# Optimization experiments

Measured on AMD Instinct MI355X. Metric: run time of the kernel, lower is better.

## Reference

```python
import jax, jax.numpy as jnp
import numpy as np

B, N, D, R = 2, 256, 128, 32

def _sh_l1(r):
    # e3nn-style component-normalized l=1 spherical harmonics of unit vectors
    return jnp.sqrt(3.0) * r

def _sh_l2(r):
    x, y, z = r[..., 0], r[..., 1], r[..., 2]
    c = jnp.sqrt(15.0)
    return jnp.stack([
        c * x * y,
        c * y * z,
        0.5 * jnp.sqrt(5.0) * (3.0 * z * z - 1.0),  # x^2+y^2+z^2 = 1
        c * x * z,
        0.5 * c * (x * x - y * y),
    ], axis=-1)

def _radial(rbf, w1, b1, w2, b2):
    h = rbf @ w1 + b1
    return (h * jax.nn.sigmoid(h)) @ w2 + b2  # Linear -> SiLU -> Linear

def _layernorm(x, g, b, eps=1e-5):
    m = jnp.mean(x, axis=-1, keepdims=True)
    v = jnp.var(x, axis=-1, keepdims=True)
    return (x - m) * jax.lax.rsqrt(v + eps) * g + b

def setup_inputs() -> dict:
    key = jax.random.key(0)
    ks = iter(jax.random.split(key, 40))
    def nrm(shape, s=1.0):
        return jax.random.normal(next(ks), shape, dtype=jnp.float32) * s
    r_hat = nrm((B, N, N, 3))
    r_hat = r_hat / (jnp.linalg.norm(r_hat, axis=-1, keepdims=True) + 1e-9)
    inp = {
        'node_s': nrm((B, N, D)),
        'node_v': nrm((B, N, 3, D)),
        'node_t': nrm((B, N, 5, D)),
        'rbf': jax.random.uniform(next(ks), (B, N, N, R), dtype=jnp.float32),
        'r_hat': r_hat,
        'mask': jnp.ones((B, N, N), dtype=jnp.float32),
    }
    s1, s2 = 1.0 / np.sqrt(R), 1.0 / np.sqrt(D)
    for p in ('r0', 'r1', 'r2', 'r110'):
        inp[p + '_w1'] = nrm((R, D), s1)
        inp[p + '_b1'] = jnp.zeros((D,), jnp.float32)
        inp[p + '_w2'] = nrm((D, D), s2)
        inp[p + '_b2'] = jnp.zeros((D,), jnp.float32)
    inp['src_w'] = nrm((D, D), s2)
    inp['ln_g'] = jnp.ones((D,), jnp.float32)
    inp['ln_b'] = jnp.zeros((D,), jnp.float32)
    inp['out_w'] = nrm((D, D), s2)
    inp['out_b'] = jnp.zeros((D,), jnp.float32)
    inp['v_scale'] = jnp.ones((D,), jnp.float32)
    inp['t_scale'] = jnp.ones((D,), jnp.float32)
    return inp

def reference(node_s, node_v, node_t, rbf, r_hat, mask,
              r0_w1, r0_b1, r0_w2, r0_b2,
              r1_w1, r1_b1, r1_w2, r1_b2,
              r2_w1, r2_b1, r2_w2, r2_b2,
              r110_w1, r110_b1, r110_w2, r110_b2,
              src_w, ln_g, ln_b, out_w, out_b, v_scale, t_scale):
    h = node_s @ src_w                               # (B,N,D)
    h_j = h[:, None, :, :] * mask[..., None]         # (B,N,N,D): h_j[b,i,j]=h[b,j]*mask[b,i,j]
    Y1 = _sh_l1(r_hat)                               # (B,N,N,3)
    Y2 = _sh_l2(r_hat)                               # (B,N,N,5)

    msg_s = jnp.sum(h_j * _radial(rbf, r0_w1, r0_b1, r0_w2, r0_b2), axis=2)  # (B,N,D)
    delta_v = jnp.einsum('bijd,bijc->bicd',
                         h_j * _radial(rbf, r1_w1, r1_b1, r1_w2, r1_b2), Y1) * v_scale
    delta_t = jnp.einsum('bijd,bijc->bicd',
                         h_j * _radial(rbf, r2_w1, r2_b1, r2_w2, r2_b2), Y2) * t_scale

    # v_j[b,i,j] = node_v[b,i] (per the torch unsqueeze(2).expand)
    dot_vY1 = jnp.einsum('bicd,bijc->bijd', node_v, Y1)                      # (B,N,N,D)
    msg_s_from_v = jnp.sum(dot_vY1 * _radial(rbf, r110_w1, r110_b1, r110_w2, r110_b2)
                           * mask[..., None], axis=2)                        # (B,N,D)

    delta_s = _layernorm(msg_s + msg_s_from_v, ln_g, ln_b) @ out_w + out_b
    return (delta_s, delta_v, delta_t)
```

## Files before the change

kernel.cpp:

```cpp
#include <hip/hip_runtime.h>

#define Bb 2
#define Nn 256
#define Dd 128
#define Rr 32

typedef unsigned short u16;
typedef unsigned int   u32;
typedef __attribute__((ext_vector_type(8))) short bf16x8;
typedef __attribute__((ext_vector_type(4))) short bf16x4;
typedef __attribute__((ext_vector_type(4))) float f32x4;
typedef __attribute__((ext_vector_type(2))) u32   u32x2;
typedef __attribute__((ext_vector_type(4))) u32   u32x4;

__device__ u16 g_w1t[4*Dd*Rr];
__device__ u16 g_w2t[4*Dd*Dd];

__device__ __forceinline__ short f2bfs(float f){
  u32 u = __float_as_uint(f);
  u += 0x7FFFu + ((u >> 16) & 1u);
  return (short)(u >> 16);
}
__device__ __forceinline__ u16 f2bf(float f){
  u32 u = __float_as_uint(f);
  u += 0x7FFFu + ((u >> 16) & 1u);
  return (u16)(u >> 16);
}
__device__ __forceinline__ u32 cvtpk(float a, float b){
  u32 r;
  asm("v_cvt_pk_bf16_f32 %0, %1, %2" : "=v"(r) : "v"(a), "v"(b));
  return r;
}
__device__ __forceinline__ int swz(int j){
  return (j&3) | ((((j>>2)^(j>>3))&1)<<2);
}

__global__ __launch_bounds__(128) void prep_kernel(
    const float* __restrict__ node_s, const float* __restrict__ src_w,
    const float* __restrict__ r0w1, const float* __restrict__ r1w1,
    const float* __restrict__ r2w1, const float* __restrict__ r3w1,
    const float* __restrict__ r0w2, const float* __restrict__ r1w2,
    const float* __restrict__ r2w2, const float* __restrict__ r3w2,
    float* __restrict__ h_out)
{
  const int bx = blockIdx.x;
  const int t  = threadIdx.x;
  if (bx < Bb*Nn){
    __shared__ float s_row[Dd];
    s_row[t] = node_s[(size_t)bx*Dd + t];
    __syncthreads();
    float acc = 0.f;
    #pragma unroll 8
    for (int k=0;k<Dd;k++) acc += s_row[k]*src_w[k*Dd + t];
    h_out[(size_t)bx*Dd + t] = acc;
  } else {
    const int kb = bx - Bb*Nn;
    const int p  = kb >> 3, sl = kb & 7;
    const float* W1 = (p==0)?r0w1:(p==1)?r1w1:(p==2)?r2w1:r3w1;
    const float* W2 = (p==0)?r0w2:(p==1)?r1w2:(p==2)?r2w2:r3w2;
    u16* W1T = g_w1t + p*Dd*Rr;
    u16* W2T = g_w2t + p*Dd*Dd;
    #pragma unroll
    for (int it=0; it<4; it++){
      int in = sl*512 + it*128 + t;
      W1T[(in & 127)*Rr + (in >> 7)] = f2bf(W1[in]);
    }
    #pragma unroll
    for (int it=0; it<16; it++){
      int in = sl*2048 + it*128 + t;
      W2T[(in & 127)*Dd + (in >> 7)] = f2bf(W2[in]);
    }
  }
}

__global__ __launch_bounds__(512,4) void se3_mfma9(
    const float* __restrict__ node_v,
    const float* __restrict__ rbf,
    const float* __restrict__ r_hat,
    const float* __restrict__ maskp,
    const float* __restrict__ r0b1, const float* __restrict__ r0b2,
    const float* __restrict__ r1b1, const float* __restrict__ r1b2,
    const float* __restrict__ r2b1, const float* __restrict__ r2b2,
    const float* __restrict__ r3b1, const float* __restrict__ r3b2,
    const float* __restrict__ ln_g, const float* __restrict__ ln_b,
    const float* __restrict__ out_w, const float* __restrict__ out_b,
    const float* __restrict__ v_scale, const float* __restrict__ t_scale,
    const float* __restrict__ h_ws,
    float* __restrict__ out_s, float* __restrict__ out_v, float* __restrict__ out_t)
{
  __shared__ u16   s_rbf[Nn*36];
  __shared__ u16   s_hid[2*64*128];
  __shared__ u16   s_YT[10*264];
  __shared__ u16   s_Y1r[3*264];
  __shared__ float s_red[16*130];
  __shared__ float s_msg[Dd];
  __shared__ float s_xn[Dd];
  __shared__ float s_part[4*Dd];
  __shared__ float s_mv[2];

  const int tid  = threadIdx.x;
  const int bi   = blockIdx.x;
  const int b    = bi >> 8;
  const int lane = tid & 63;
  const int w    = tid >> 6;
  const int q    = lane >> 4;
  const int cc   = lane & 15;
  const int mpair= w & 1;
  const int dgrp = w >> 1;
  const int dbase= dgrp*32;

  if (tid < Nn){
    int j = tid;
    size_t pidx = (size_t)bi*Nn + j;
    float mk = maskp[pidx];
    float x = r_hat[pidx*3+0];
    float y = r_hat[pidx*3+1];
    float z = r_hat[pidx*3+2];
    const float SQ3=1.7320508075688772f;
    const float C15=3.8729833462074170f;
    const float C5H=1.1180339887498949f;
    float y1a=SQ3*x, y1b=SQ3*y, y1c=SQ3*z;
    s_YT[0*264+j]=f2bf(mk);
    s_YT[1*264+j]=f2bf(y1a*mk);
    s_YT[2*264+j]=f2bf(y1b*mk);
    s_YT[3*264+j]=f2bf(y1c*mk);
    s_YT[4*264+j]=f2bf(C15*x*y*mk);
    s_YT[5*264+j]=f2bf(C15*y*z*mk);
    s_YT[6*264+j]=f2bf(C5H*(3.f*z*z-1.f)*mk);
    s_YT[7*264+j]=f2bf(C15*x*z*mk);
    s_YT[8*264+j]=f2bf(0.5f*C15*(x*x-y*y)*mk);
    s_YT[9*264+j]=f2bf(mk);
    s_Y1r[0*264+j]=f2bf(y1a);
    s_Y1r[1*264+j]=f2bf(y1b);
    s_Y1r[2*264+j]=f2bf(y1c);
  }

  const float* rbf_blk = rbf + (size_t)bi*Nn*Rr;
  const float* hb      = h_ws + (size_t)b*Nn*Dd;

  for (int idx=tid; idx<Nn*Rr/2; idx+=512){
    int j = idx >> 4, r2 = (idx & 15)*2;
    const float* src = &rbf_blk[j*Rr + r2];
    float v0 = src[0], v1 = src[1];
    *(u32*)&s_rbf[j*36 + r2] = cvtpk(v0, v1);
  }

  bf16x8 vBf[2];
  {
    const float* nv = node_v + (size_t)bi*3*Dd;
    #pragma unroll
    for (int nt=0;nt<2;nt++){
      int dd = dbase+nt*16+cc;
      bf16x8 t = {0,0,0,0,0,0,0,0};
      if (q==0){
        t[0]=f2bfs(nv[0*Dd+dd]);
        t[1]=f2bfs(nv[1*Dd+dd]);
        t[2]=f2bfs(nv[2*Dd+dd]);
      }
      vBf[nt]=t;
    }
  }

  __syncthreads();

  const f32x4 zf = {0.f,0.f,0.f,0.f};
  f32x4 accred[2] = {zf, zf};
  int buf = 0;

  #pragma unroll 1
  for (int p=0;p<4;p++){
    const float* B1p = (p==0)?r0b1:(p==1)?r1b1:(p==2)?r2b1:r3b1;
    const float* B2p = (p==0)?r0b2:(p==1)?r1b2:(p==2)?r2b2:r3b2;
    const u16* W1T = g_w1t + p*Dd*Rr;
    const u16* W2T = g_w2t + p*Dd*Dd;
    const int lo = (p==0)?0:(p==1)?1:(p==2)?4:9;
    const int hi = (p==0)?0:(p==1)?3:(p==2)?8:9;
    const u32 gmask = (cc>=lo && cc<=hi) ? 0xFFFFFFFFu : 0u;
    const u16* ytrow = &s_YT[(cc<10?cc:9)*264];

    bf16x8 w1f[2];
    bf16x8 w2f[2][4];
    f32x4  b1v4[2];
    float  b2v[2];
    #pragma unroll
    for (int nt=0;nt<2;nt++){
      int dd = dbase+nt*16+cc;
      b1v4[nt] = *(const f32x4*)&B1p[dbase + nt*16 + q*4];
      b2v[nt]=B2p[dd];
      w1f[nt] = *(const bf16x8*)&W1T[dd*Rr + q*8];
      #pragma unroll
      for (int ks=0;ks<4;ks++)
        w2f[nt][ks] = *(const bf16x8*)&W2T[dd*Dd + ks*32 + q*8];
    }

    #pragma unroll 1
    for (int ch=0; ch<4; ch++){
      #pragma unroll
      for (int jt=0;jt<2;jt++){
        const int jrow = (mpair*2+jt)*16 + cc;
        const u16* bp = &s_rbf[(ch*64 + jrow)*36 + q*8];
        bf16x4 lo4 = *(const bf16x4*)bp;
        bf16x4 hi4 = *(const bf16x4*)(bp+4);
        bf16x8 rbff = {lo4[0],lo4[1],lo4[2],lo4[3],hi4[0],hi4[1],hi4[2],hi4[3]};
        #pragma unroll
        for (int nt=0;nt<2;nt++){
          f32x4 hc = __builtin_amdgcn_mfma_f32_16x16x32_bf16(w1f[nt], rbff, zf, 0,0,0);
          float s[4];
          #pragma unroll
          for (int r=0;r<4;r++){
            float x  = hc[r] + b1v4[nt][r];
            float e  = __expf(-x);
            s[r]     = x*__builtin_amdgcn_rcpf(1.f+e);
          }
          u32x2 pk = { cvtpk(s[0], s[1]), cvtpk(s[2], s[3]) };
          const int c0 = dgrp*4 + nt*2 + (q>>1);
          *(u32x2*)&s_hid[buf*8192 + jrow*128 + ((c0 ^ swz(jrow))<<3) + (q&1)*4] = pk;
        }
      }
      __syncthreads();

      u32 bB[2][4];
      #pragma unroll
      for (int mm=0;mm<2;mm++){
        const int jp = mpair*32 + ((cc>>2)<<3) + mm*4 + (cc&3);
        bf16x8 af[4];
        #pragma unroll
        for (int ks=0;ks<4;ks++)
          af[ks] = *(const bf16x8*)&s_hid[buf*8192 + jp*128 + (((ks*4+q) ^ swz(jp))<<3)];

        f32x4 dotC[2];
        if (p==3){
          bf16x8 aY = {0,0,0,0,0,0,0,0};
          if (q==0){
            int jg = ch*64 + jp;
            aY[0]=(short)s_Y1r[0*264+jg];
            aY[1]=(short)s_Y1r[1*264+jg];
            aY[2]=(short)s_Y1r[2*264+jg];
          }
          #pragma unroll
          for (int nt=0;nt<2;nt++)
            dotC[nt] = __builtin_amdgcn_mfma_f32_16x16x32_bf16(aY, vBf[nt], zf, 0,0,0);
        }

        #pragma unroll
        for (int nt=0;nt<2;nt++){
          f32x4 c2 = zf;
          #pragma unroll
          for (int ks=0;ks<4;ks++)
            c2 = __builtin_amdgcn_mfma_f32_16x16x32_bf16(af[ks], w2f[nt][ks], c2, 0,0,0);
          const int dd = dbase+nt*16+cc;
          float g[4];
          if (p<3){
            const float* hp = hb + (size_t)(ch*64 + mpair*32 + q*8 + mm*4)*Dd + dd;
            #pragma unroll
            for (int r=0;r<4;r++)
              g[r] = (c2[r]+b2v[nt]) * hp[(size_t)r*Dd];
          } else {
            #pragma unroll
            for (int r=0;r<4;r++)
              g[r] = (c2[r]+b2v[nt]) * dotC[nt][r];
          }
          bB[nt][mm*2+0] = cvtpk(g[0], g[1]);
          bB[nt][mm*2+1] = cvtpk(g[2], g[3]);
        }
      }

      {
        bf16x8 aR = *(const bf16x8*)(ytrow + ch*64 + mpair*32 + q*8);
        u32* arp = (u32*)&aR;
        arp[0]&=gmask; arp[1]&=gmask; arp[2]&=gmask; arp[3]&=gmask;
        #pragma unroll
        for (int nt=0;nt<2;nt++){
          u32x4 bw = { bB[nt][0], bB[nt][1], bB[nt][2], bB[nt][3] };
          bf16x8 bG = __builtin_bit_cast(bf16x8, bw);
          accred[nt] = __builtin_amdgcn_mfma_f32_16x16x32_bf16(aR, bG, accred[nt], 0,0,0);
        }
      }
      buf ^= 1;
    }
  }

  if (mpair){
    #pragma unroll
    for (int nt=0;nt<2;nt++){
      const int d = dbase + nt*16 + cc;
      #pragma unroll
      for (int r=0;r<4;r++)
        s_red[(q*4+r)*130 + d] = accred[nt][r];
    }
  }
  __syncthreads();
  if (!mpair){
    #pragma unroll
    for (int nt=0;nt<2;nt++){
      const int d = dbase + nt*16 + cc;
      #pragma unroll
      for (int r=0;r<4;r++){
        const int rw = q*4 + r;
        float val = accred[nt][r] + s_red[rw*130 + d];
        if (rw==0)      s_msg[d] = val;
        else if (rw<=3) out_v[(size_t)bi*3*Dd + (size_t)(rw-1)*Dd + d] = val*v_scale[d];
        else if (rw<=8) out_t[(size_t)bi*5*Dd + (size_t)(rw-4)*Dd + d] = val*t_scale[d];
        else if (rw==9) s_xn[d] = val;
      }
    }
  }
  __syncthreads();

  if (tid < 64){
    float a0=s_msg[tid]+s_xn[tid], a1=s_msg[tid+64]+s_xn[tid+64];
    float s1=a0+a1, s2=a0*a0+a1*a1;
    #pragma unroll
    for (int off=1;off<64;off<<=1){
      s1 += __shfl_xor(s1,off);
      s2 += __shfl_xor(s2,off);
    }
    if (tid==0){
      float m   = s1*(1.f/Dd);
      float var = fmaxf(s2*(1.f/Dd) - m*m, 0.f);
      s_mv[0]=m;
      s_mv[1]=rsqrtf(var+1e-5f);
    }
  }
  __syncthreads();
  if (tid < Dd){
    float msg = s_msg[tid]+s_xn[tid];
    s_xn[tid] = (msg - s_mv[0])*s_mv[1]*ln_g[tid] + ln_b[tid];
  }
  __syncthreads();

  {
    int dp = tid & 127, seg = tid >> 7;
    float pa = 0.f;
    #pragma unroll 8
    for (int k=seg*32;k<seg*32+32;k++)
      pa += s_xn[k]*out_w[k*Dd+dp];
    s_part[seg*Dd+dp]=pa;
  }
  __syncthreads();
  if (tid < Dd)
    out_s[(size_t)bi*Dd+tid] = s_part[tid]+s_part[Dd+tid]+s_part[2*Dd+tid]+s_part[3*Dd+tid]+out_b[tid];
}

extern "C" void kernel_launch(void* const* d_in, const int* in_sizes, int n_in,
                              void* d_out, int out_size, void* d_ws, size_t ws_size,
                              hipStream_t stream) {
  const float* node_s = (const float*)d_in[0];
  const float* node_v = (const float*)d_in[1];
  const float* rbf    = (const float*)d_in[3];
  const float* r_hat  = (const float*)d_in[4];
  const float* maskp  = (const float*)d_in[5];
  const float* r0w1=(const float*)d_in[6],  *r0b1=(const float*)d_in[7];
  const float* r0w2=(const float*)d_in[8],  *r0b2=(const float*)d_in[9];
  const float* r1w1=(const float*)d_in[10], *r1b1=(const float*)d_in[11];
  const float* r1w2=(const float*)d_in[12], *r1b2=(const float*)d_in[13];
  const float* r2w1=(const float*)d_in[14], *r2b1=(const float*)d_in[15];
  const float* r2w2=(const float*)d_in[16], *r2b2=(const float*)d_in[17];
  const float* r3w1=(const float*)d_in[18], *r3b1=(const float*)d_in[19];
  const float* r3w2=(const float*)d_in[20], *r3b2=(const float*)d_in[21];
  const float* src_w  =(const float*)d_in[22];
  const float* ln_g   =(const float*)d_in[23];
  const float* ln_b   =(const float*)d_in[24];
  const float* out_w  =(const float*)d_in[25];
  const float* out_b  =(const float*)d_in[26];
  const float* v_scale=(const float*)d_in[27];
  const float* t_scale=(const float*)d_in[28];

  float* h_ws = (float*)d_ws;
  float* out_s = (float*)d_out;
  float* out_v = out_s + (size_t)Bb*Nn*Dd;
  float* out_t = out_v + (size_t)Bb*Nn*3*Dd;

  prep_kernel<<<dim3(Bb*Nn + 32), dim3(128), 0, stream>>>(
      node_s, src_w,
      r0w1, r1w1, r2w1, r3w1, r0w2, r1w2, r2w2, r3w2,
      h_ws);
  se3_mfma9<<<dim3(Bb*Nn), dim3(512), 0, stream>>>(
      node_v, rbf, r_hat, maskp,
      r0b1,r0b2, r1b1,r1b2, r2b1,r2b2, r3b1,r3b2,
      ln_g, ln_b, out_w, out_b, v_scale, t_scale,
      h_ws, out_s, out_v, out_t);
}
```

Measured before the change: 192.0 us.

## Shrink block to 256 threads, drop j-split reduction and double-buffered hidden tile

The main kernel now uses 4 waves instead of 8. Each wave covers a 32-wide d-slice and walks all 64 j-rows of each chunk itself, so the j split across wave pairs goes away and with it the cross-wave shared-memory reduction. The hidden-activation buffer is single-buffered, with a sync added at the start of each chunk. The final-stage scratch arrays alias that buffer, and the l=1 harmonics for the p==3 path are recomputed from global r_hat instead of being staged in shared memory. This cuts shared memory and sync overhead to allow more resident blocks, at the cost of fewer waves per block, less in-block parallelism, and the loss of overlap between chunks.

Result: slower. 212.3 us (+10.6%).

```diff
diff --git a/kernel.cpp b/kernel.cpp
--- a/kernel.cpp
+++ b/kernel.cpp
@@ -73,7 +73,9 @@
   }
 }
 
-__global__ __launch_bounds__(512,4) void se3_mfma9(
+__global__ __launch_bounds__(256)
+__attribute__((amdgpu_waves_per_eu(4,4)))
+void se3_mfma10(
     const float* __restrict__ node_v,
     const float* __restrict__ rbf,
     const float* __restrict__ r_hat,
@@ -88,15 +90,13 @@
     const float* __restrict__ h_ws,
     float* __restrict__ out_s, float* __restrict__ out_v, float* __restrict__ out_t)
 {
-  __shared__ u16   s_rbf[Nn*36];
-  __shared__ u16   s_hid[2*64*128];
-  __shared__ u16   s_YT[10*264];
-  __shared__ u16   s_Y1r[3*264];
-  __shared__ float s_red[16*130];
-  __shared__ float s_msg[Dd];
-  __shared__ float s_xn[Dd];
-  __shared__ float s_part[4*Dd];
-  __shared__ float s_mv[2];
+  __shared__ u16 s_rbf[Nn*36];
+  __shared__ u16 s_hid[64*128];
+  __shared__ u16 s_YT[10*264];
+  float* s_msg  = (float*)s_hid;
+  float* s_xn   = s_msg + Dd;
+  float* s_part = s_xn  + Dd;
+  float* s_mv   = s_part + 2*Dd;
 
   const int tid  = threadIdx.x;
   const int bi   = blockIdx.x;
@@ -105,11 +105,9 @@
   const int w    = tid >> 6;
   const int q    = lane >> 4;
   const int cc   = lane & 15;
-  const int mpair= w & 1;
-  const int dgrp = w >> 1;
-  const int dbase= dgrp*32;
-
-  if (tid < Nn){
+  const int dbase= w*32;
+
+  {
     int j = tid;
     size_t pidx = (size_t)bi*Nn + j;
     float mk = maskp[pidx];
@@ -119,26 +117,23 @@
     const float SQ3=1.7320508075688772f;
     const float C15=3.8729833462074170f;
     const float C5H=1.1180339887498949f;
-    float y1a=SQ3*x, y1b=SQ3*y, y1c=SQ3*z;
     s_YT[0*264+j]=f2bf(mk);
-    s_YT[1*264+j]=f2bf(y1a*mk);
-    s_YT[2*264+j]=f2bf(y1b*mk);
-    s_YT[3*264+j]=f2bf(y1c*mk);
+    s_YT[1*264+j]=f2bf(SQ3*x*mk);
+    s_YT[2*264+j]=f2bf(SQ3*y*mk);
+    s_YT[3*264+j]=f2bf(SQ3*z*mk);
     s_YT[4*264+j]=f2bf(C15*x*y*mk);
     s_YT[5*264+j]=f2bf(C15*y*z*mk);
     s_YT[6*264+j]=f2bf(C5H*(3.f*z*z-1.f)*mk);
     s_YT[7*264+j]=f2bf(C15*x*z*mk);
     s_YT[8*264+j]=f2bf(0.5f*C15*(x*x-y*y)*mk);
     s_YT[9*264+j]=f2bf(mk);
-    s_Y1r[0*264+j]=f2bf(y1a);
-    s_Y1r[1*264+j]=f2bf(y1b);
-    s_Y1r[2*264+j]=f2bf(y1c);
   }
 
   const float* rbf_blk = rbf + (size_t)bi*Nn*Rr;
+  const float* rh_blk  = r_hat + (size_t)bi*Nn*3;
   const float* hb      = h_ws + (size_t)b*Nn*Dd;
 
-  for (int idx=tid; idx<Nn*Rr/2; idx+=512){
+  for (int idx=tid; idx<Nn*Rr/2; idx+=256){
     int j = idx >> 4, r2 = (idx & 15)*2;
     const float* src = &rbf_blk[j*Rr + r2];
     float v0 = src[0], v1 = src[1];
@@ -161,11 +156,9 @@
     }
   }
 
-  __syncthreads();
-
   const f32x4 zf = {0.f,0.f,0.f,0.f};
   f32x4 accred[2] = {zf, zf};
-  int buf = 0;
+  const u16* ytrow = &s_YT[(cc<10?cc:9)*264];
 
   #pragma unroll 1
   for (int p=0;p<4;p++){
@@ -176,7 +169,6 @@
     const int lo = (p==0)?0:(p==1)?1:(p==2)?4:9;
     const int hi = (p==0)?0:(p==1)?3:(p==2)?8:9;
     const u32 gmask = (cc>=lo && cc<=hi) ? 0xFFFFFFFFu : 0u;
-    const u16* ytrow = &s_YT[(cc<10?cc:9)*264];
 
     bf16x8 w1f[2];
     bf16x8 w2f[2][4];
@@ -195,9 +187,10 @@
 
     #pragma unroll 1
     for (int ch=0; ch<4; ch++){
-      #pragma unroll
-      for (int jt=0;jt<2;jt++){
-        const int jrow = (mpair*2+jt)*16 + cc;
+      __syncthreads();
+      #pragma unroll 1
+      for (int jt=0;jt<4;jt++){
+        const int jrow = jt*16 + cc;
         const u16* bp = &s_rbf[(ch*64 + jrow)*36 + q*8];
         bf16x4 lo4 = *(const bf16x4*)bp;
         bf16x4 hi4 = *(const bf16x4*)(bp+4);
@@ -213,60 +206,61 @@
             s[r]     = x*__builtin_amdgcn_rcpf(1.f+e);
           }
           u32x2 pk = { cvtpk(s[0], s[1]), cvtpk(s[2], s[3]) };
-          const int c0 = dgrp*4 + nt*2 + (q>>1);
-          *(u32x2*)&s_hid[buf*8192 + jrow*128 + ((c0 ^ swz(jrow))<<3) + (q&1)*4] = pk;
+          const int c0 = w*4 + nt*2 + (q>>1);
+          *(u32x2*)&s_hid[jrow*128 + ((c0 ^ swz(jrow))<<3) + (q&1)*4] = pk;
         }
       }
       __syncthreads();
 
-      u32 bB[2][4];
-      #pragma unroll
-      for (int mm=0;mm<2;mm++){
-        const int jp = mpair*32 + ((cc>>2)<<3) + mm*4 + (cc&3);
-        bf16x8 af[4];
-        #pragma unroll
-        for (int ks=0;ks<4;ks++)
-          af[ks] = *(const bf16x8*)&s_hid[buf*8192 + jp*128 + (((ks*4+q) ^ swz(jp))<<3)];
-
-        f32x4 dotC[2];
-        if (p==3){
-          bf16x8 aY = {0,0,0,0,0,0,0,0};
-          if (q==0){
-            int jg = ch*64 + jp;
-            aY[0]=(short)s_Y1r[0*264+jg];
-            aY[1]=(short)s_Y1r[1*264+jg];
-            aY[2]=(short)s_Y1r[2*264+jg];
-          }
-          #pragma unroll
-          for (int nt=0;nt<2;nt++)
-            dotC[nt] = __builtin_amdgcn_mfma_f32_16x16x32_bf16(aY, vBf[nt], zf, 0,0,0);
-        }
-
-        #pragma unroll
-        for (int nt=0;nt<2;nt++){
-          f32x4 c2 = zf;
+      #pragma unroll 1
+      for (int g=0; g<2; g++){
+        u32 bB[2][4];
+        #pragma unroll 1
+        for (int mm=0;mm<2;mm++){
+          const int jp = g*32 + ((cc>>2)<<3) + mm*4 + (cc&3);
+          bf16x8 af[4];
           #pragma unroll
           for (int ks=0;ks<4;ks++)
-            c2 = __builtin_amdgcn_mfma_f32_16x16x32_bf16(af[ks], w2f[nt][ks], c2, 0,0,0);
-          const int dd = dbase+nt*16+cc;
-          float g[4];
-          if (p<3){
-            const float* hp = hb + (size_t)(ch*64 + mpair*32 + q*8 + mm*4)*Dd + dd;
+            af[ks] = *(const bf16x8*)&s_hid[jp*128 + (((ks*4+q) ^ swz(jp))<<3)];
+
+          f32x4 dotC[2];
+          if (p==3){
+            bf16x8 aY = {0,0,0,0,0,0,0,0};
+            if (q==0){
+              const float SQ3=1.7320508075688772f;
+              const float* rh = &rh_blk[(size_t)(ch*64 + jp)*3];
+              aY[0]=f2bfs(SQ3*rh[0]);
+              aY[1]=f2bfs(SQ3*rh[1]);
+              aY[2]=f2bfs(SQ3*rh[2]);
+            }
             #pragma unroll
-            for (int r=0;r<4;r++)
-              g[r] = (c2[r]+b2v[nt]) * hp[(size_t)r*Dd];
-          } else {
+            for (int nt=0;nt<2;nt++)
+              dotC[nt] = __builtin_amdgcn_mfma_f32_16x16x32_bf16(aY, vBf[nt], zf, 0,0,0);
+          }
+
+          #pragma unroll
+          for (int nt=0;nt<2;nt++){
+            f32x4 c2 = zf;
             #pragma unroll
-            for (int r=0;r<4;r++)
-              g[r] = (c2[r]+b2v[nt]) * dotC[nt][r];
+            for (int ks=0;ks<4;ks++)
+              c2 = __builtin_amdgcn_mfma_f32_16x16x32_bf16(af[ks], w2f[nt][ks], c2, 0,0,0);
+            const int dd = dbase+nt*16+cc;
+            float gg[4];
+            if (p<3){
+              const float* hp = hb + (size_t)(ch*64 + g*32 + q*8 + mm*4)*Dd + dd;
+              #pragma unroll
+              for (int r=0;r<4;r++)
+                gg[r] = (c2[r]+b2v[nt]) * hp[(size_t)r*Dd];
+            } else {
+              #pragma unroll
+              for (int r=0;r<4;r++)
+                gg[r] = (c2[r]+b2v[nt]) * dotC[nt][r];
+            }
+            bB[nt][mm*2+0] = cvtpk(gg[0], gg[1]);
+            bB[nt][mm*2+1] = cvtpk(gg[2], gg[3]);
           }
-          bB[nt][mm*2+0] = cvtpk(g[0], g[1]);
-          bB[nt][mm*2+1] = cvtpk(g[2], g[3]);
         }
-      }
-
-      {
-        bf16x8 aR = *(const bf16x8*)(ytrow + ch*64 + mpair*32 + q*8);
+        bf16x8 aR = *(const bf16x8*)(ytrow + ch*64 + g*32 + q*8);
         u32* arp = (u32*)&aR;
         arp[0]&=gmask; arp[1]&=gmask; arp[2]&=gmask; arp[3]&=gmask;
         #pragma unroll
@@ -276,33 +270,22 @@
           accred[nt] = __builtin_amdgcn_mfma_f32_16x16x32_bf16(aR, bG, accred[nt], 0,0,0);
         }
       }
-      buf ^= 1;
-    }
-  }
-
-  if (mpair){
-    #pragma unroll
-    for (int nt=0;nt<2;nt++){
-      const int d = dbase + nt*16 + cc;
-      #pragma unroll
-      for (int r=0;r<4;r++)
-        s_red[(q*4+r)*130 + d] = accred[nt][r];
-    }
-  }
-  __syncthreads();
-  if (!mpair){
-    #pragma unroll
-    for (int nt=0;nt<2;nt++){
-      const int d = dbase + nt*16 + cc;
-      #pragma unroll
-      for (int r=0;r<4;r++){
-        const int rw = q*4 + r;
-        float val = accred[nt][r] + s_red[rw*130 + d];
-        if (rw==0)      s_msg[d] = val;
-        else if (rw<=3) out_v[(size_t)bi*3*Dd + (size_t)(rw-1)*Dd + d] = val*v_scale[d];
-        else if (rw<=8) out_t[(size_t)bi*5*Dd + (size_t)(rw-4)*Dd + d] = val*t_scale[d];
-        else if (rw==9) s_xn[d] = val;
-      }
+    }
+  }
+
+  __syncthreads();
+
+  #pragma unroll
+  for (int nt=0;nt<2;nt++){
+    const int d = dbase + nt*16 + cc;
+    #pragma unroll
+    for (int r=0;r<4;r++){
+      const int rw = q*4 + r;
+      float val = accred[nt][r];
+      if (rw==0)      s_msg[d] = val;
+      else if (rw<=3) out_v[(size_t)bi*3*Dd + (size_t)(rw-1)*Dd + d] = val*v_scale[d];
+      else if (rw<=8) out_t[(size_t)bi*5*Dd + (size_t)(rw-4)*Dd + d] = val*t_scale[d];
+      else if (rw==9) s_xn[d] = val;
     }
   }
   __syncthreads();
@@ -333,13 +316,13 @@
     int dp = tid & 127, seg = tid >> 7;
     float pa = 0.f;
     #pragma unroll 8
-    for (int k=seg*32;k<seg*32+32;k++)
+    for (int k=seg*64;k<seg*64+64;k++)
       pa += s_xn[k]*out_w[k*Dd+dp];
     s_part[seg*Dd+dp]=pa;
   }
   __syncthreads();
   if (tid < Dd)
-    out_s[(size_t)bi*Dd+tid] = s_part[tid]+s_part[Dd+tid]+s_part[2*Dd+tid]+s_part[3*Dd+tid]+out_b[tid];
+    out_s[(size_t)bi*Dd+tid] = s_part[tid]+s_part[Dd+tid]+out_b[tid];
 }
 
 extern "C" void kernel_launch(void* const* d_in, const int* in_sizes, int n_in,
@@ -375,7 +358,7 @@
       node_s, src_w,
       r0w1, r1w1, r2w1, r3w1, r0w2, r1w2, r2w2, r3w2,
       h_ws);
-  se3_mfma9<<<dim3(Bb*Nn), dim3(512), 0, stream>>>(
+  se3_mfma10<<<dim3(Bb*Nn), dim3(256), 0, stream>>>(
       node_v, rbf, r_hat, maskp,
       r0b1,r0b2, r1b1,r1b2, r2b1,r2b2, r3b1,r3b2,
       ln_g, ln_b, out_w, out_b, v_scale, t_scale,
```
